# Optimization experiments

Measured on AMD Instinct MI355X. Metric: run time of the kernel, lower is better.

The kernel has to match this reference:

```python
import jax, jax.numpy as jnp
import numpy as np

HC = 4
C = 2048
TMAX = 8
RMS_EPS = 1e-6
PRE_EPS = 1e-4
SINK_EPS = 1e-6
POST_MULT = 2.0


def setup_inputs() -> dict:
    key = jax.random.key(0)
    k1, k2, k3 = jax.random.split(key, 3)
    B, S = 2, 2048
    x = jax.random.normal(k1, (B, S, HC, C), dtype=jnp.float32)
    phi = jax.random.normal(k2, (HC * C, HC * HC + 2 * HC), dtype=jnp.float32) * 0.02
    b = jnp.zeros((HC * HC + 2 * HC,), dtype=jnp.float32)
    alpha_pre = jnp.ones((), dtype=jnp.float32)
    alpha_post = jnp.ones((), dtype=jnp.float32)
    alpha_res = jnp.ones((), dtype=jnp.float32)
    W = jax.random.normal(k3, (C, C), dtype=jnp.float32) * 0.02
    Wb = jnp.zeros((C,), dtype=jnp.float32)
    return {"x": x, "phi": phi, "b": b, "alpha_pre": alpha_pre,
            "alpha_post": alpha_post, "alpha_res": alpha_res, "W": W, "Wb": Wb}


def _coeffs(x, phi, b, alpha_pre, alpha_post, alpha_res):
    # x: [..., hc, c] -> flatten streams, RMSNorm over k = hc*c
    lead = x.shape[:-2]
    flat = x.reshape(lead + (HC * C,))
    xn = flat * jax.lax.rsqrt(jnp.mean(flat * flat, axis=-1, keepdims=True) + RMS_EPS)
    logits = xn @ phi + b  # [..., hc*hc + 2*hc]
    pre = logits[..., :HC]
    post = logits[..., HC:2 * HC]
    res = logits[..., 2 * HC:].reshape(lead + (HC, HC))
    h_pre = jax.nn.sigmoid(alpha_pre * pre) + PRE_EPS          # [..., hc]
    h_post = POST_MULT * jax.nn.sigmoid(alpha_post * post)     # [..., hc]
    # Sinkhorn normalization -> approximately doubly-stochastic hc x hc matrix
    M = jnp.exp(alpha_res * res)

    def step(m, _):
        m = m / (jnp.sum(m, axis=-1, keepdims=True) + SINK_EPS)
        m = m / (jnp.sum(m, axis=-2, keepdims=True) + SINK_EPS)
        return m, None

    h_res, _ = jax.lax.scan(step, M, None, length=TMAX)
    return h_pre, h_post, h_res


def reference(x, phi, b, alpha_pre, alpha_post, alpha_res, W, Wb):
    xf = x.astype(jnp.float32)
    h_pre, h_post, h_res = _coeffs(xf, phi, b, alpha_pre, alpha_post, alpha_res)
    # combine streams into single layer input: [..., c]
    x_in = jnp.sum(xf * h_pre[..., None], axis=-2)
    f_out = x_in @ W + Wb  # the wrapped layer (Linear)
    # residual stream mixing + broadcasted post-scaled layer output
    x_out = jnp.einsum('...oi,...ic->...oc', h_res, xf) + h_post[..., None] * f_out[..., None, :]
    return x_out.astype(x.dtype)
```

## Files before the change

### kernel.cpp

```cpp
#include <hip/hip_runtime.h>
#include <hip/hip_bf16.h>

#define HCn 4
#define Cn 2048
#define Dn (HCn*Cn)
#define NLg 24
#define TMAXn 8

typedef short bf16x8 __attribute__((ext_vector_type(8)));
typedef float f32x4 __attribute__((ext_vector_type(4)));

__device__ __forceinline__ unsigned int pk2(float a, float b) {
  union { __hip_bfloat162 h; unsigned int u; } v;
  v.h = __float22bfloat162_rn(float2{a, b});
  return v.u;
}
__device__ __forceinline__ float sigm(float z) { return 1.0f / (1.0f + expf(-z)); }

__device__ __forceinline__ void gload_lds16(const void* g, void* l) {
  __builtin_amdgcn_global_load_lds((__attribute__((address_space(1))) void*)(g),
                                   (__attribute__((address_space(3))) void*)(l),
                                   16, 0, 0);
}

__global__ __launch_bounds__(128) void phib_kernel(const float* __restrict__ phi,
                                                   unsigned short* __restrict__ phiB) {
  int tid = threadIdx.x;
  int nt = tid >> 6, lane = tid & 63;
  int ks = blockIdx.x;
  int col = nt * 16 + (lane & 15);
  int kb = ks * 32 + (lane >> 4) * 8;
  float v[8];
#pragma unroll
  for (int e = 0; e < 8; ++e)
    v[e] = (col < NLg) ? phi[(size_t)(kb + e) * NLg + col] : 0.f;
  uint4 o = { pk2(v[0], v[1]), pk2(v[2], v[3]), pk2(v[4], v[5]), pk2(v[6], v[7]) };
  *(uint4*)&phiB[((size_t)(ks * 2 + nt) * 64 + lane) * 8] = o;
}

__global__ __launch_bounds__(512) void coeffs_kernel(
    const float* __restrict__ x, const unsigned short* __restrict__ phiB,
    const float* __restrict__ bb, const float* __restrict__ apre_p,
    const float* __restrict__ apost_p, const float* __restrict__ ares_p,
    unsigned int* __restrict__ xin, float* __restrict__ hpost, float* __restrict__ hres) {
  __shared__ __align__(16) unsigned short As[8][2][1024];
  __shared__ float lgp[8][16][33];
  __shared__ float ssp[8][16];
  __shared__ float hpre_s[16][HCn];

  int tid = threadIdx.x, lane = tid & 63, wid = tid >> 6;
  long t0 = (long)blockIdx.x * 16;
  const float* xblk = x + (size_t)t0 * Dn;

  int srow = lane >> 2;
  const float* xw = xblk + (size_t)srow * Dn + wid * 1024 + (lane & 3) * 16;
  int wb0 = srow * 128 + (((lane & 3) * 32) ^ ((srow & 7) << 4));
  int wb1 = srow * 128 + (((lane & 3) * 32 + 16) ^ ((srow & 7) << 4));
  int rrow = lane & 15;
  int rb0 = rrow * 128 + (((lane >> 4) * 16) ^ ((rrow & 7) << 4));
  int rb1 = rrow * 128 + ((64 + (lane >> 4) * 16) ^ ((rrow & 7) << 4));

  const bf16x8* pB0 = (const bf16x8*)phiB + (size_t)wid * 4096 + lane;

  float ss = 0.f;
  f32x4 acc0 = {0.f, 0.f, 0.f, 0.f}, acc1 = {0.f, 0.f, 0.f, 0.f};

#define LOADB(IT, B) { int j2 = (IT) * 2;                 \
    B[0] = pB0[(j2 * 2 + 0) * 64];                        \
    B[1] = pB0[(j2 * 2 + 1) * 64];                        \
    B[2] = pB0[((j2 + 1) * 2 + 0) * 64];                  \
    B[3] = pB0[((j2 + 1) * 2 + 1) * 64]; }

#define STAGE(IT, BUF) {                                                      \
    const float4* sp_ = (const float4*)(xw + (IT) * 64);                      \
    float4 v0 = sp_[0], v1 = sp_[1], v2 = sp_[2], v3 = sp_[3];                \
    ss += v0.x*v0.x + v0.y*v0.y + v0.z*v0.z + v0.w*v0.w;                      \
    ss += v1.x*v1.x + v1.y*v1.y + v1.z*v1.z + v1.w*v1.w;                      \
    ss += v2.x*v2.x + v2.y*v2.y + v2.z*v2.z + v2.w*v2.w;                      \
    ss += v3.x*v3.x + v3.y*v3.y + v3.z*v3.z + v3.w*v3.w;                      \
    uint4 lo = { pk2(v0.x,v0.y), pk2(v0.z,v0.w), pk2(v1.x,v1.y), pk2(v1.z,v1.w) }; \
    uint4 hi = { pk2(v2.x,v2.y), pk2(v2.z,v2.w), pk2(v3.x,v3.y), pk2(v3.z,v3.w) }; \
    *(uint4*)((char*)(BUF) + wb0) = lo;                                       \
    *(uint4*)((char*)(BUF) + wb1) = hi; }

#define MFMASTEP(BUF, B) {                                                    \
    bf16x8 a0 = *(const bf16x8*)((char*)(BUF) + rb0);                         \
    bf16x8 a1 = *(const bf16x8*)((char*)(BUF) + rb1);                         \
    acc0 = __builtin_amdgcn_mfma_f32_16x16x32_bf16(a0, B[0], acc0, 0, 0, 0);  \
    acc1 = __builtin_amdgcn_mfma_f32_16x16x32_bf16(a0, B[1], acc1, 0, 0, 0);  \
    acc0 = __builtin_amdgcn_mfma_f32_16x16x32_bf16(a1, B[2], acc0, 0, 0, 0);  \
    acc1 = __builtin_amdgcn_mfma_f32_16x16x32_bf16(a1, B[3], acc1, 0, 0, 0); }

  unsigned short* A0 = &As[wid][0][0];
  unsigned short* A1 = &As[wid][1][0];
  bf16x8 bA[4], bB[4];
  LOADB(0, bA); STAGE(0, A0);
#pragma unroll
  for (int ii = 0; ii < 8; ++ii) {
    LOADB(ii * 2 + 1, bB); STAGE(ii * 2 + 1, A1);
    MFMASTEP(A0, bA);
    if (ii < 7) { LOADB(ii * 2 + 2, bA); STAGE(ii * 2 + 2, A0); }
    MFMASTEP(A1, bB);
  }
#undef LOADB
#undef STAGE
#undef MFMASTEP

  ss += __shfl_xor(ss, 1); ss += __shfl_xor(ss, 2);
  if ((lane & 3) == 0) ssp[wid][srow] = ss;
#pragma unroll
  for (int e = 0; e < 4; ++e) {
    int row = (lane >> 4) * 4 + e;
    lgp[wid][row][lane & 15] = acc0[e];
    lgp[wid][row][16 + (lane & 15)] = acc1[e];
  }
  __syncthreads();

  if (tid < 16) {
    long t = t0 + tid;
    float st = 0.f;
#pragma unroll
    for (int w = 0; w < 8; ++w) st += ssp[w][tid];
    float r = rsqrtf(st / (float)Dn + 1e-6f);
    float apre = apre_p[0], apost = apost_p[0], ares = ares_p[0];
    float lg[NLg];
#pragma unroll
    for (int j = 0; j < NLg; ++j) {
      float d = 0.f;
#pragma unroll
      for (int w = 0; w < 8; ++w) d += lgp[w][tid][j];
      lg[j] = r * d + bb[j];
    }
#pragma unroll
    for (int j = 0; j < 4; ++j) hpre_s[tid][j] = sigm(apre * lg[j]) + 1e-4f;
#pragma unroll
    for (int j = 0; j < 4; ++j) hpost[t * 4 + j] = 2.0f * sigm(apost * lg[4 + j]);
    float m[16];
#pragma unroll
    for (int q = 0; q < 16; ++q) m[q] = expf(ares * lg[8 + q]);
    for (int it = 0; it < TMAXn; ++it) {
#pragma unroll
      for (int o = 0; o < 4; ++o) {
        float rs = m[o*4] + m[o*4+1] + m[o*4+2] + m[o*4+3] + 1e-6f;
        m[o*4] /= rs; m[o*4+1] /= rs; m[o*4+2] /= rs; m[o*4+3] /= rs;
      }
#pragma unroll
      for (int i = 0; i < 4; ++i) {
        float cs = m[i] + m[4+i] + m[8+i] + m[12+i] + 1e-6f;
        m[i] /= cs; m[4+i] /= cs; m[8+i] /= cs; m[12+i] /= cs;
      }
    }
#pragma unroll
    for (int q = 0; q < 16; ++q) hres[t * 16 + q] = m[q];
  }
  __syncthreads();

  int t = tid >> 5, l32 = tid & 31;
  const float4* xt = (const float4*)(xblk + (size_t)t * Dn);
  float h0 = hpre_s[t][0], h1 = hpre_s[t][1], h2 = hpre_s[t][2], h3 = hpre_s[t][3];
  uint2* xo = (uint2*)xin + (size_t)(t0 + t) * (Cn / 4);
#pragma unroll
  for (int itc = 0; itc < 16; ++itc) {
    int c4 = itc * 32 + l32;
    float4 v0 = xt[c4];
    float4 v1 = xt[c4 + 512];
    float4 v2 = xt[c4 + 1024];
    float4 v3 = xt[c4 + 1536];
    float sx = h0*v0.x + h1*v1.x + h2*v2.x + h3*v3.x;
    float sy = h0*v0.y + h1*v1.y + h2*v2.y + h3*v3.y;
    float sz = h0*v0.z + h1*v1.z + h2*v2.z + h3*v3.z;
    float sw = h0*v0.w + h1*v1.w + h2*v2.w + h3*v3.w;
    uint2 o; o.x = pk2(sx, sy); o.y = pk2(sz, sw);
    xo[c4] = o;
  }
}

__global__ __launch_bounds__(256) void wtrans_kernel(const float* __restrict__ W,
                                                     unsigned short* __restrict__ Wt) {
  __shared__ float tile[64][65];
  int kb = blockIdx.y * 64, nb = blockIdx.x * 64;
  int tr = threadIdx.x >> 4;
  int tc = threadIdx.x & 15;
#pragma unroll
  for (int rr = 0; rr < 64; rr += 16) {
    float4 v = *(const float4*)&W[(size_t)(kb + tr + rr) * Cn + nb + tc * 4];
    tile[tr + rr][tc * 4 + 0] = v.x; tile[tr + rr][tc * 4 + 1] = v.y;
    tile[tr + rr][tc * 4 + 2] = v.z; tile[tr + rr][tc * 4 + 3] = v.w;
  }
  __syncthreads();
#pragma unroll
  for (int rr = 0; rr < 64; rr += 16) {
    int n = nb + tr + rr;
    uint2 o;
    o.x = pk2(tile[tc * 4 + 0][tr + rr], tile[tc * 4 + 1][tr + rr]);
    o.y = pk2(tile[tc * 4 + 2][tr + rr], tile[tc * 4 + 3][tr + rr]);
    *(uint2*)&Wt[(size_t)n * Cn + kb + tc * 4] = o;
  }
}

#define BMt 128
#define BNt 128
#define BKt 32
#define GK Cn
__global__ __launch_bounds__(256) void gemm_ep_kernel(
    const unsigned short* __restrict__ xin, const unsigned short* __restrict__ Wt,
    const float* __restrict__ x, const float* __restrict__ Wb,
    const float* __restrict__ hpost, const float* __restrict__ hres,
    float* __restrict__ out) {
  __shared__ __align__(16) unsigned short As[BMt * BKt];
  __shared__ __align__(16) unsigned short Bs[BNt * BKt];
  int tid = threadIdx.x;
  int lane = tid & 63, wid = tid >> 6;
  int wr = wid >> 1, wc = wid & 1;
  int l15 = lane & 15, l4 = lane >> 4;
  int bx = blockIdx.x, by = blockIdx.y;

  f32x4 acc[4][4];
#pragma unroll
  for (int i = 0; i < 4; ++i)
#pragma unroll
    for (int j = 0; j < 4; ++j) acc[i][j] = {0.f, 0.f, 0.f, 0.f};

  const char* Ab = (const char*)xin + (size_t)by * BMt * GK * 2;
  const char* Bb = (const char*)Wt + (size_t)bx * BNt * GK * 2;
  int off0 = tid * 16, off1 = tid * 16 + 4096;
  int row0 = off0 >> 6, colb0 = off0 & 63;
  int row1 = off1 >> 6, colb1 = off1 & 63;

  for (int k0 = 0; k0 < GK; k0 += BKt) {
    gload_lds16(Ab + (size_t)row0 * (GK * 2) + k0 * 2 + colb0, (char*)As + off0);
    gload_lds16(Ab + (size_t)row1 * (GK * 2) + k0 * 2 + colb1, (char*)As + off1);
    gload_lds16(Bb + (size_t)row0 * (GK * 2) + k0 * 2 + colb0, (char*)Bs + off0);
    gload_lds16(Bb + (size_t)row1 * (GK * 2) + k0 * 2 + colb1, (char*)Bs + off1);
    __syncthreads();
    bf16x8 af[4], bfv[4];
#pragma unroll
    for (int fm = 0; fm < 4; ++fm)
      af[fm] = *(const bf16x8*)&As[(wr * 64 + fm * 16 + l15) * BKt + l4 * 8];
#pragma unroll
    for (int fn = 0; fn < 4; ++fn)
      bfv[fn] = *(const bf16x8*)&Bs[(wc * 64 + fn * 16 + l15) * BKt + l4 * 8];
#pragma unroll
    for (int fm = 0; fm < 4; ++fm)
#pragma unroll
      for (int fn = 0; fn < 4; ++fn)
        acc[fm][fn] = __builtin_amdgcn_mfma_f32_16x16x32_bf16(af[fm], bfv[fn], acc[fm][fn], 0, 0, 0);
    __syncthreads();
  }

  int m0 = by * BMt + wr * 64;
  int n0 = bx * BNt + wc * 64;
#pragma unroll
  for (int fm = 0; fm < 4; ++fm) {
#pragma unroll
    for (int e = 0; e < 4; ++e) {
      int t = m0 + fm * 16 + l4 * 4 + e;
      const float* hr = hres + (size_t)t * 16;
      const float* hq = hpost + (size_t)t * 4;
      const float* xt = x + (size_t)t * Dn;
      float* ot = out + (size_t)t * Dn;
      float hr_[16], hq_[4];
#pragma unroll
      for (int q = 0; q < 16; ++q) hr_[q] = hr[q];
#pragma unroll
      for (int q = 0; q < 4; ++q) hq_[q] = hq[q];
#pragma unroll
      for (int fn = 0; fn < 4; ++fn) {
        int c = n0 + fn * 16 + l15;
        float f = acc[fm][fn][e] + Wb[c];
        float x0 = xt[c], x1 = xt[Cn + c], x2 = xt[2 * Cn + c], x3 = xt[3 * Cn + c];
#pragma unroll
        for (int o = 0; o < 4; ++o) {
          ot[(size_t)o * Cn + c] =
              hq_[o] * f + hr_[o*4+0] * x0 + hr_[o*4+1] * x1 + hr_[o*4+2] * x2 + hr_[o*4+3] * x3;
        }
      }
    }
  }
}

extern "C" void kernel_launch(void* const* d_in, const int* in_sizes, int n_in,
                              void* d_out, int out_size, void* d_ws, size_t ws_size,
                              hipStream_t stream) {
  const float* x     = (const float*)d_in[0];
  const float* phi   = (const float*)d_in[1];
  const float* b     = (const float*)d_in[2];
  const float* apre  = (const float*)d_in[3];
  const float* apost = (const float*)d_in[4];
  const float* ares  = (const float*)d_in[5];
  const float* W     = (const float*)d_in[6];
  const float* Wb    = (const float*)d_in[7];
  float* out = (float*)d_out;

  int NT = in_sizes[0] / Dn;
  char* ws = (char*)d_ws;
  size_t xin_b = (size_t)NT * Cn * 2;
  size_t wt_b  = (size_t)Cn * Cn * 2;
  size_t hp_b  = (size_t)NT * 4 * 4;
  size_t hr_b  = (size_t)NT * 16 * 4;
  unsigned int*   xin  = (unsigned int*)ws;
  unsigned short* Wt   = (unsigned short*)(ws + xin_b);
  float* hpost = (float*)(ws + xin_b + wt_b);
  float* hres  = (float*)(ws + xin_b + wt_b + hp_b);
  unsigned short* phiB = (unsigned short*)(ws + xin_b + wt_b + hp_b + hr_b);

  hipLaunchKernelGGL(phib_kernel, dim3(Dn / 32), dim3(128), 0, stream, phi, phiB);
  hipLaunchKernelGGL(coeffs_kernel, dim3(NT / 16), dim3(512), 0, stream,
                     x, phiB, b, apre, apost, ares, xin, hpost, hres);
  hipLaunchKernelGGL(wtrans_kernel, dim3(Cn / 64, Cn / 64), dim3(256), 0, stream, W, Wt);
  hipLaunchKernelGGL(gemm_ep_kernel, dim3(Cn / BNt, NT / BMt), dim3(256), 0, stream,
                     (const unsigned short*)xin, Wt, x, Wb, hpost, hres, out);
}
```

Baseline: 186.7 us.

## Feed MFMA A-operand directly from registers and remap GEMM blocks across XCDs

The coeffs kernel no longer stages x through swizzled LDS buffers. Each lane now loads the 8 contiguous floats it needs straight into the bf16 MFMA A-fragment layout, with a two-deep register prefetch, which removes LDS writes and reads and the associated waits. The phiB indexing and the sum-of-squares shuffle reduction are adjusted to match the new token/k lane mapping. Separately, the GEMM launch becomes a 1D grid whose block index is remapped in groups of eight, likely to match the round-robin dispatch of workgroups to XCDs and improve L2 reuse. The remap hardcodes a 16x32 tile grid, so it depends on the current problem size.

```diff
diff --git a/kernel.cpp b/kernel.cpp
--- a/kernel.cpp
+++ b/kernel.cpp
@@ -43,7 +43,6 @@
     const float* __restrict__ bb, const float* __restrict__ apre_p,
     const float* __restrict__ apost_p, const float* __restrict__ ares_p,
     unsigned int* __restrict__ xin, float* __restrict__ hpost, float* __restrict__ hres) {
-  __shared__ __align__(16) unsigned short As[8][2][1024];
   __shared__ float lgp[8][16][33];
   __shared__ float ssp[8][16];
   __shared__ float hpre_s[16][HCn];
@@ -52,67 +51,48 @@
   long t0 = (long)blockIdx.x * 16;
   const float* xblk = x + (size_t)t0 * Dn;
 
-  int srow = lane >> 2;
-  const float* xw = xblk + (size_t)srow * Dn + wid * 1024 + (lane & 3) * 16;
-  int wb0 = srow * 128 + (((lane & 3) * 32) ^ ((srow & 7) << 4));
-  int wb1 = srow * 128 + (((lane & 3) * 32 + 16) ^ ((srow & 7) << 4));
-  int rrow = lane & 15;
-  int rb0 = rrow * 128 + (((lane >> 4) * 16) ^ ((rrow & 7) << 4));
-  int rb1 = rrow * 128 + ((64 + (lane >> 4) * 16) ^ ((rrow & 7) << 4));
-
-  const bf16x8* pB0 = (const bf16x8*)phiB + (size_t)wid * 4096 + lane;
+  int l15 = lane & 15, kg = lane >> 4;
+  const float* xr = xblk + (size_t)l15 * Dn + wid * 1024 + kg * 8;
+  const bf16x8* pB = (const bf16x8*)phiB + (size_t)wid * 32 * 128 + lane;
 
   float ss = 0.f;
-  f32x4 acc0 = {0.f, 0.f, 0.f, 0.f}, acc1 = {0.f, 0.f, 0.f, 0.f};
-
-#define LOADB(IT, B) { int j2 = (IT) * 2;                 \
-    B[0] = pB0[(j2 * 2 + 0) * 64];                        \
-    B[1] = pB0[(j2 * 2 + 1) * 64];                        \
-    B[2] = pB0[((j2 + 1) * 2 + 0) * 64];                  \
-    B[3] = pB0[((j2 + 1) * 2 + 1) * 64]; }
-
-#define STAGE(IT, BUF) {                                                      \
-    const float4* sp_ = (const float4*)(xw + (IT) * 64);                      \
-    float4 v0 = sp_[0], v1 = sp_[1], v2 = sp_[2], v3 = sp_[3];                \
-    ss += v0.x*v0.x + v0.y*v0.y + v0.z*v0.z + v0.w*v0.w;                      \
-    ss += v1.x*v1.x + v1.y*v1.y + v1.z*v1.z + v1.w*v1.w;                      \
-    ss += v2.x*v2.x + v2.y*v2.y + v2.z*v2.z + v2.w*v2.w;                      \
-    ss += v3.x*v3.x + v3.y*v3.y + v3.z*v3.z + v3.w*v3.w;                      \
-    uint4 lo = { pk2(v0.x,v0.y), pk2(v0.z,v0.w), pk2(v1.x,v1.y), pk2(v1.z,v1.w) }; \
-    uint4 hi = { pk2(v2.x,v2.y), pk2(v2.z,v2.w), pk2(v3.x,v3.y), pk2(v3.z,v3.w) }; \
-    *(uint4*)((char*)(BUF) + wb0) = lo;                                       \
-    *(uint4*)((char*)(BUF) + wb1) = hi; }
-
-#define MFMASTEP(BUF, B) {                                                    \
-    bf16x8 a0 = *(const bf16x8*)((char*)(BUF) + rb0);                         \
-    bf16x8 a1 = *(const bf16x8*)((char*)(BUF) + rb1);                         \
-    acc0 = __builtin_amdgcn_mfma_f32_16x16x32_bf16(a0, B[0], acc0, 0, 0, 0);  \
-    acc1 = __builtin_amdgcn_mfma_f32_16x16x32_bf16(a0, B[1], acc1, 0, 0, 0);  \
-    acc0 = __builtin_amdgcn_mfma_f32_16x16x32_bf16(a1, B[2], acc0, 0, 0, 0);  \
-    acc1 = __builtin_amdgcn_mfma_f32_16x16x32_bf16(a1, B[3], acc1, 0, 0, 0); }
-
-  unsigned short* A0 = &As[wid][0][0];
-  unsigned short* A1 = &As[wid][1][0];
-  bf16x8 bA[4], bB[4];
-  LOADB(0, bA); STAGE(0, A0);
-#pragma unroll
-  for (int ii = 0; ii < 8; ++ii) {
-    LOADB(ii * 2 + 1, bB); STAGE(ii * 2 + 1, A1);
-    MFMASTEP(A0, bA);
-    if (ii < 7) { LOADB(ii * 2 + 2, bA); STAGE(ii * 2 + 2, A0); }
-    MFMASTEP(A1, bB);
-  }
-#undef LOADB
-#undef STAGE
-#undef MFMASTEP
-
-  ss += __shfl_xor(ss, 1); ss += __shfl_xor(ss, 2);
-  if ((lane & 3) == 0) ssp[wid][srow] = ss;
+  f32x4 acc0 = {0.f,0.f,0.f,0.f}, acc1 = {0.f,0.f,0.f,0.f};
+
+#define LOADIT(IT, P0, P1, B0, B1) {            \
+    P0 = *(const float4*)(xr + (IT) * 32);      \
+    P1 = *(const float4*)(xr + (IT) * 32 + 4);  \
+    B0 = pB[(IT) * 128];                        \
+    B1 = pB[(IT) * 128 + 64]; }
+
+#define PROCIT(P0, P1, B0, B1) {                                              \
+    ss += P0.x*P0.x + P0.y*P0.y + P0.z*P0.z + P0.w*P0.w;                      \
+    ss += P1.x*P1.x + P1.y*P1.y + P1.z*P1.z + P1.w*P1.w;                      \
+    uint4 u_ = { pk2(P0.x,P0.y), pk2(P0.z,P0.w), pk2(P1.x,P1.y), pk2(P1.z,P1.w) }; \
+    bf16x8 a_ = *(bf16x8*)&u_;                                                \
+    acc0 = __builtin_amdgcn_mfma_f32_16x16x32_bf16(a_, B0, acc0, 0, 0, 0);    \
+    acc1 = __builtin_amdgcn_mfma_f32_16x16x32_bf16(a_, B1, acc1, 0, 0, 0); }
+
+  {
+    float4 pA0, pA1, qA0, qA1; bf16x8 bA0, bA1, bB0, bB1;
+    LOADIT(0, pA0, pA1, bA0, bA1);
+#pragma unroll
+    for (int it = 0; it < 32; it += 2) {
+      LOADIT(it + 1, qA0, qA1, bB0, bB1);
+      PROCIT(pA0, pA1, bA0, bA1);
+      if (it + 2 < 32) LOADIT(it + 2, pA0, pA1, bA0, bA1);
+      PROCIT(qA0, qA1, bB0, bB1);
+    }
+  }
+#undef LOADIT
+#undef PROCIT
+
+  ss += __shfl_xor(ss, 16); ss += __shfl_xor(ss, 32);
+  if (kg == 0) ssp[wid][l15] = ss;
 #pragma unroll
   for (int e = 0; e < 4; ++e) {
-    int row = (lane >> 4) * 4 + e;
-    lgp[wid][row][lane & 15] = acc0[e];
-    lgp[wid][row][16 + (lane & 15)] = acc1[e];
+    int tok = kg * 4 + e;
+    lgp[wid][tok][l15] = acc0[e];
+    lgp[wid][tok][16 + l15] = acc1[e];
   }
   __syncthreads();
 
@@ -213,7 +193,9 @@
   int lane = tid & 63, wid = tid >> 6;
   int wr = wid >> 1, wc = wid & 1;
   int l15 = lane & 15, l4 = lane >> 4;
-  int bx = blockIdx.x, by = blockIdx.y;
+  int wg = blockIdx.x;
+  wg = (wg & 7) * 64 + (wg >> 3);
+  int bx = wg & 15, by = wg >> 4;
 
   f32x4 acc[4][4];
 #pragma unroll
@@ -308,6 +290,6 @@
   hipLaunchKernelGGL(coeffs_kernel, dim3(NT / 16), dim3(512), 0, stream,
                      x, phiB, b, apre, apost, ares, xin, hpost, hres);
   hipLaunchKernelGGL(wtrans_kernel, dim3(Cn / 64, Cn / 64), dim3(256), 0, stream, W, Wt);
-  hipLaunchKernelGGL(gemm_ep_kernel, dim3(Cn / BNt, NT / BMt), dim3(256), 0, stream,
+  hipLaunchKernelGGL(gemm_ep_kernel, dim3((Cn / BNt) * (NT / BMt)), dim3(256), 0, stream,
                      (const unsigned short*)xin, Wt, x, Wb, hpost, hres, out);
 }
```

Result: faster. 177.8 us (-4.8%).
